# Optimization experiments

Hardware: AMD Instinct MI355X
Metric: run time of the kernel (lower is better)

## Reference

```python
import jax, jax.numpy as jnp
from jax import lax
import numpy as np


def setup_inputs() -> dict:
    key = jax.random.key(0)
    k1, k2 = jax.random.split(key)
    x = jax.random.normal(k1, (128, 256, 3), dtype=jnp.float32)
    y = jax.random.normal(k2, (128, 256, 3), dtype=jnp.float32)
    return {"x": x, "y": y}


def _frechet(x, y):
    B, n, _ = x.shape
    m = y.shape[1]
    INF = jnp.float32(jnp.inf)
    # pairwise squared-distance cost: (B, n, m)
    cost = jnp.sum((x[:, :, None, :] - y[:, None, :, :]) ** 2, axis=-1)

    # DP row 0: dist[0,0]=0, dist[0,j>0]=inf
    row0 = jnp.full((B, m + 1), INF, dtype=cost.dtype).at[:, 0].set(0.0)

    def row_step(prev_row, cost_row):
        # prev_row: (B, m+1) = dist[i-1, :]; cost_row: (B, m)
        up = prev_row[:, 1:]     # dist[i-1, j]   for j=1..m -> (B, m)
        diag = prev_row[:, :-1]  # dist[i-1, j-1] -> (B, m)

        def col_step(left, inp):
            c, u, d = inp  # each (B,)
            min_prev = jnp.minimum(jnp.minimum(u, left), d)
            # torch.where(cost > min_prev, cost, min_prev) == max(cost, min_prev)
            val = jnp.maximum(c, min_prev)
            return val, val

        init_left = jnp.full((B,), INF, dtype=cost.dtype)  # dist[i, 0] = inf
        _, vals = lax.scan(col_step, init_left,
                           (cost_row.T, up.T, diag.T))  # vals: (m, B)
        cur_row = jnp.concatenate(
            [jnp.full((B, 1), INF, dtype=cost.dtype), vals.T], axis=1)
        return cur_row, None

    last_row, _ = lax.scan(row_step, row0, jnp.moveaxis(cost, 1, 0))
    return last_row[:, -1]  # dist[:, n, m] -> (B,)


def reference(x, y):
    return _frechet(x, y)
```

## Files before the change

### kernel.cpp

```cpp
#include <hip/hip_runtime.h>

#define N 256
#define LANES 64
#define NPAIRS 264
#define PPAD   64

typedef float f32x2 __attribute__((ext_vector_type(2)));
typedef float f32x4 __attribute__((ext_vector_type(4)));

__device__ __forceinline__ float dpp_shr1_inf(float v) {
    return __int_as_float(__builtin_amdgcn_update_dpp(
        0x7f800000, __float_as_int(v), 0x138 , 0xf, 0xf, false));
}

__global__ __launch_bounds__(64) void frechet_lin(
    const float* __restrict__ x,
    const float* __restrict__ y,
    float* __restrict__ out)
{
    const int b = blockIdx.x;
    const int t = threadIdx.x;

    const float INF = __builtin_inff();

    __shared__ f32x4 ldsY[2 * NPAIRS];

    {
        const f32x4 pad0 = {0.0f, 0.0f, 0.0f, 0.0f};
        const f32x4 pad1 = {0.0f, 0.0f, INF, INF};
        ldsY[2 * t]     = pad0;
        ldsY[2 * t + 1] = pad1;
        for (int pp = 192 + t; pp < NPAIRS; pp += 64) {
            ldsY[2 * pp]     = pad0;
            ldsY[2 * pp + 1] = pad1;
        }
    }

    #pragma unroll
    for (int k = 0; k < 2; ++k) {
        const int pr = t + 64 * k;
        const int base = (b * N + 2 * pr) * 3;
        const float a0x = y[base + 0], a0y = y[base + 1], a0z = y[base + 2];
        const float a1x = y[base + 3], a1y = y[base + 4], a1z = y[base + 5];
        const float ss0 = a0x*a0x + a0y*a0y + a0z*a0z;
        const float ss1 = a1x*a1x + a1y*a1y + a1z*a1z;
        const int p = pr + PPAD;
        const f32x4 w0 = {a0x, a1x, a0y, a1y};
        const f32x4 w1 = {a0z, a1z, ss0, ss1};
        ldsY[2 * p]     = w0;
        ldsY[2 * p + 1] = w1;
    }

    f32x2 xp0[4], xp1[4], xp2[4], sxp[4];
    #pragma unroll
    for (int r = 0; r < 4; ++r) {
        const float a0 = x[(b * N + 4 * t + r) * 3 + 0];
        const float a1 = x[(b * N + 4 * t + r) * 3 + 1];
        const float a2 = x[(b * N + 4 * t + r) * 3 + 2];
        const float m0 = -2.0f * a0, m1 = -2.0f * a1, m2 = -2.0f * a2;
        const float s  = a0 * a0 + a1 * a1 + a2 * a2;
        xp0[r].x = m0; xp0[r].y = m0;
        xp1[r].x = m1; xp1[r].y = m1;
        xp2[r].x = m2; xp2[r].y = m2;
        sxp[r].x = s;  sxp[r].y = s;
    }
    __syncthreads();

    float lv0 = INF, lv1 = INF, lv2 = INF, lv3 = INF;
    float cb0 = INF, cb1 = INF;
    float diagv = (t == 0) ? 0.0f : INF;

    #define STEP(Q0, Q1)                                                          \
    {                                                                             \
        const float u0 = dpp_shr1_inf(cb0);                                       \
        const float u1 = dpp_shr1_inf(cb1);                                       \
        const f32x2 y0p = (Q0).xy, y1p = (Q0).zw;                                 \
        const f32x2 y2p = (Q1).xy, sab = (Q1).zw;                                 \
        const f32x2 c0p = __builtin_elementwise_fma(xp0[0], y0p,                  \
                          __builtin_elementwise_fma(xp1[0], y1p,                  \
                          __builtin_elementwise_fma(xp2[0], y2p, sxp[0] + sab))); \
        const f32x2 c1p = __builtin_elementwise_fma(xp0[1], y0p,                  \
                          __builtin_elementwise_fma(xp1[1], y1p,                  \
                          __builtin_elementwise_fma(xp2[1], y2p, sxp[1] + sab))); \
        const f32x2 c2p = __builtin_elementwise_fma(xp0[2], y0p,                  \
                          __builtin_elementwise_fma(xp1[2], y1p,                  \
                          __builtin_elementwise_fma(xp2[2], y2p, sxp[2] + sab))); \
        const f32x2 c3p = __builtin_elementwise_fma(xp0[3], y0p,                  \
                          __builtin_elementwise_fma(xp1[3], y1p,                  \
                          __builtin_elementwise_fma(xp2[3], y2p, sxp[3] + sab))); \
        const float v0 = fmaxf(c0p.x, fminf(fminf(u0, lv0), diagv));              \
        const float v1 = fmaxf(c1p.x, fminf(fminf(v0, lv1), lv0));                \
        const float v2 = fmaxf(c2p.x, fminf(fminf(v1, lv2), lv1));                \
        const float v3 = fmaxf(c3p.x, fminf(fminf(v2, lv3), lv2));                \
        const float w0 = fmaxf(c0p.y, fminf(fminf(u1, v0), u0));                  \
        const float w1 = fmaxf(c1p.y, fminf(fminf(w0, v1), v0));                  \
        const float w2 = fmaxf(c2p.y, fminf(fminf(w1, v2), v1));                  \
        const float w3 = fmaxf(c3p.y, fminf(fminf(w2, v3), v2));                  \
        lv0 = w0; lv1 = w1; lv2 = w2; lv3 = w3;                                   \
        cb0 = v3; cb1 = w3;                                                       \
        diagv = u1;                                                               \
    }

    const int q0 = PPAD - t;
    const f32x4* bp = &ldsY[2 * q0];
    f32x4 yA0 = bp[0], yA1 = bp[1];
    f32x4 yB0 = bp[2], yB1 = bp[3];
    f32x4 yC0 = bp[4], yC1 = bp[5];
    bp += 6;

    #pragma unroll 3
    for (int k = 0; k < 63; ++k) {
        STEP(yA0, yA1); yA0 = bp[0]; yA1 = bp[1];
        STEP(yB0, yB1); yB0 = bp[2]; yB1 = bp[3];
        STEP(yC0, yC1); yC0 = bp[4]; yC1 = bp[5];
        bp += 6;
    }
    STEP(yA0, yA1);
    STEP(yB0, yB1);

    #undef STEP

    if (t == LANES - 1)
        out[b] = cb1;
}

extern "C" void kernel_launch(void* const* d_in, const int* in_sizes, int n_in,
                              void* d_out, int out_size, void* d_ws, size_t ws_size,
                              hipStream_t stream) {
    const float* x = (const float*)d_in[0];
    const float* y = (const float*)d_in[1];
    float* out = (float*)d_out;

    const int B = in_sizes[0] / (N * 3);
    frechet_lin<<<B, LANES, 0, stream>>>(x, y, out);
}
```

Measured before the change: 21.38 us.

## Split Frechet DP into forward and reverse wavefronts meeting at anti-diagonal

```diff
diff --git a/kernel.cpp b/kernel.cpp
--- a/kernel.cpp
+++ b/kernel.cpp
@@ -2,8 +2,9 @@
 
 #define N 256
 #define LANES 64
-#define NPAIRS 264
-#define PPAD   64
+#define FRONT 128
+#define NPAIRS 260
+#define NSTEP 128
 
 typedef float f32x2 __attribute__((ext_vector_type(2)));
 typedef float f32x4 __attribute__((ext_vector_type(4)));
@@ -13,50 +14,62 @@
         0x7f800000, __float_as_int(v), 0x138 , 0xf, 0xf, false));
 }
 
-__global__ __launch_bounds__(64) void frechet_lin(
+__global__ __launch_bounds__(128) void frechet_bidir(
     const float* __restrict__ x,
     const float* __restrict__ y,
     float* __restrict__ out)
 {
-    const int b = blockIdx.x;
-    const int t = threadIdx.x;
+    const int b   = blockIdx.x;
+    const int tid = threadIdx.x;
+    const int wid = tid >> 6;
+    const int t   = tid & 63;
 
     const float INF = __builtin_inff();
 
-    __shared__ f32x4 ldsY[2 * NPAIRS];
+    __shared__ f32x4 ldsY[2][2 * NPAIRS];
+    __shared__ float Fd253[256], Fd254[256], Rd254[256], Rd255[256];
+
+    f32x4* reg = ldsY[wid];
 
     {
         const f32x4 pad0 = {0.0f, 0.0f, 0.0f, 0.0f};
         const f32x4 pad1 = {0.0f, 0.0f, INF, INF};
-        ldsY[2 * t]     = pad0;
-        ldsY[2 * t + 1] = pad1;
-        for (int pp = 192 + t; pp < NPAIRS; pp += 64) {
-            ldsY[2 * pp]     = pad0;
-            ldsY[2 * pp + 1] = pad1;
+        reg[2 * t]            = pad0;  reg[2 * t + 1]            = pad1;
+        reg[2 * (t + 64)]     = pad0;  reg[2 * (t + 64) + 1]     = pad1;
+        if (t < 4) {
+            const int pp = FRONT + 128 + t;
+            reg[2 * pp] = pad0;  reg[2 * pp + 1] = pad1;
         }
     }
 
     #pragma unroll
     for (int k = 0; k < 2; ++k) {
         const int pr = t + 64 * k;
-        const int base = (b * N + 2 * pr) * 3;
-        const float a0x = y[base + 0], a0y = y[base + 1], a0z = y[base + 2];
-        const float a1x = y[base + 3], a1y = y[base + 4], a1z = y[base + 5];
+        const int c0 = 2 * pr, c1 = 2 * pr + 1;
+        const int oc0 = wid ? (255 - c0) : c0;
+        const int oc1 = wid ? (255 - c1) : c1;
+        const float a0x = y[(b * N + oc0) * 3 + 0];
+        const float a0y = y[(b * N + oc0) * 3 + 1];
+        const float a0z = y[(b * N + oc0) * 3 + 2];
+        const float a1x = y[(b * N + oc1) * 3 + 0];
+        const float a1y = y[(b * N + oc1) * 3 + 1];
+        const float a1z = y[(b * N + oc1) * 3 + 2];
         const float ss0 = a0x*a0x + a0y*a0y + a0z*a0z;
         const float ss1 = a1x*a1x + a1y*a1y + a1z*a1z;
-        const int p = pr + PPAD;
+        const int p = FRONT + pr;
         const f32x4 w0 = {a0x, a1x, a0y, a1y};
         const f32x4 w1 = {a0z, a1z, ss0, ss1};
-        ldsY[2 * p]     = w0;
-        ldsY[2 * p + 1] = w1;
+        reg[2 * p]     = w0;
+        reg[2 * p + 1] = w1;
     }
 
     f32x2 xp0[4], xp1[4], xp2[4], sxp[4];
     #pragma unroll
     for (int r = 0; r < 4; ++r) {
-        const float a0 = x[(b * N + 4 * t + r) * 3 + 0];
-        const float a1 = x[(b * N + 4 * t + r) * 3 + 1];
-        const float a2 = x[(b * N + 4 * t + r) * 3 + 2];
+        const int orow = wid ? (255 - (4 * t + r)) : (4 * t + r);
+        const float a0 = x[(b * N + orow) * 3 + 0];
+        const float a1 = x[(b * N + orow) * 3 + 1];
+        const float a2 = x[(b * N + orow) * 3 + 2];
         const float m0 = -2.0f * a0, m1 = -2.0f * a1, m2 = -2.0f * a2;
         const float s  = a0 * a0 + a1 * a1 + a2 * a2;
         xp0[r].x = m0; xp0[r].y = m0;
@@ -67,61 +80,97 @@
     __syncthreads();
 
     float lv0 = INF, lv1 = INF, lv2 = INF, lv3 = INF;
-    float cb0 = INF, cb1 = INF;
+    float g0 = INF, g1 = INF;
+    float h0 = INF, h1 = INF;
     float diagv = (t == 0) ? 0.0f : INF;
+    float V0, V1, V2, V3, W0, W1, W2, W3;
 
-    #define STEP(Q0, Q1)                                                          \
-    {                                                                             \
-        const float u0 = dpp_shr1_inf(cb0);                                       \
-        const float u1 = dpp_shr1_inf(cb1);                                       \
-        const f32x2 y0p = (Q0).xy, y1p = (Q0).zw;                                 \
-        const f32x2 y2p = (Q1).xy, sab = (Q1).zw;                                 \
-        const f32x2 c0p = __builtin_elementwise_fma(xp0[0], y0p,                  \
-                          __builtin_elementwise_fma(xp1[0], y1p,                  \
+    #define STEP(Q0v, Q1v, Y0, Y1)                                            \
+    {                                                                         \
+        const float u0 = dpp_shr1_inf(Q0v);                                   \
+        const float u1 = dpp_shr1_inf(Q1v);                                   \
+        const f32x2 y0p = (Y0).xy, y1p = (Y0).zw;                             \
+        const f32x2 y2p = (Y1).xy, sab = (Y1).zw;                             \
+        const f32x2 c0p = __builtin_elementwise_fma(xp0[0], y0p,              \
+                          __builtin_elementwise_fma(xp1[0], y1p,              \
                           __builtin_elementwise_fma(xp2[0], y2p, sxp[0] + sab))); \
-        const f32x2 c1p = __builtin_elementwise_fma(xp0[1], y0p,                  \
-                          __builtin_elementwise_fma(xp1[1], y1p,                  \
+        const f32x2 c1p = __builtin_elementwise_fma(xp0[1], y0p,              \
+                          __builtin_elementwise_fma(xp1[1], y1p,              \
                           __builtin_elementwise_fma(xp2[1], y2p, sxp[1] + sab))); \
-        const f32x2 c2p = __builtin_elementwise_fma(xp0[2], y0p,                  \
-                          __builtin_elementwise_fma(xp1[2], y1p,                  \
+        const f32x2 c2p = __builtin_elementwise_fma(xp0[2], y0p,              \
+                          __builtin_elementwise_fma(xp1[2], y1p,              \
                           __builtin_elementwise_fma(xp2[2], y2p, sxp[2] + sab))); \
-        const f32x2 c3p = __builtin_elementwise_fma(xp0[3], y0p,                  \
-                          __builtin_elementwise_fma(xp1[3], y1p,                  \
+        const f32x2 c3p = __builtin_elementwise_fma(xp0[3], y0p,              \
+                          __builtin_elementwise_fma(xp1[3], y1p,              \
                           __builtin_elementwise_fma(xp2[3], y2p, sxp[3] + sab))); \
-        const float v0 = fmaxf(c0p.x, fminf(fminf(u0, lv0), diagv));              \
-        const float v1 = fmaxf(c1p.x, fminf(fminf(v0, lv1), lv0));                \
-        const float v2 = fmaxf(c2p.x, fminf(fminf(v1, lv2), lv1));                \
-        const float v3 = fmaxf(c3p.x, fminf(fminf(v2, lv3), lv2));                \
-        const float w0 = fmaxf(c0p.y, fminf(fminf(u1, v0), u0));                  \
-        const float w1 = fmaxf(c1p.y, fminf(fminf(w0, v1), v0));                  \
-        const float w2 = fmaxf(c2p.y, fminf(fminf(w1, v2), v1));                  \
-        const float w3 = fmaxf(c3p.y, fminf(fminf(w2, v3), v2));                  \
-        lv0 = w0; lv1 = w1; lv2 = w2; lv3 = w3;                                   \
-        cb0 = v3; cb1 = w3;                                                       \
-        diagv = u1;                                                               \
+        V0 = fmaxf(c0p.x, fminf(fminf(u0, lv0), diagv));                      \
+        V1 = fmaxf(c1p.x, fminf(fminf(V0, lv1), lv0));                        \
+        V2 = fmaxf(c2p.x, fminf(fminf(V1, lv2), lv1));                        \
+        V3 = fmaxf(c3p.x, fminf(fminf(V2, lv3), lv2));                        \
+        W0 = fmaxf(c0p.y, fminf(fminf(u1, V0), u0));                          \
+        W1 = fmaxf(c1p.y, fminf(fminf(W0, V1), V0));                          \
+        W2 = fmaxf(c2p.y, fminf(fminf(W1, V2), V1));                          \
+        W3 = fmaxf(c3p.y, fminf(fminf(W2, V3), V2));                          \
+        lv0 = W0; lv1 = W1; lv2 = W2; lv3 = W3;                               \
+        Q0v = V3; Q1v = W3;                                                   \
+        diagv = u1;                                                           \
     }
 
-    const int q0 = PPAD - t;
-    const f32x4* bp = &ldsY[2 * q0];
+    const int q0 = FRONT - 2 * t;
+    const f32x4* bp = &reg[2 * q0];
     f32x4 yA0 = bp[0], yA1 = bp[1];
     f32x4 yB0 = bp[2], yB1 = bp[3];
     f32x4 yC0 = bp[4], yC1 = bp[5];
     bp += 6;
 
-    #pragma unroll 3
-    for (int k = 0; k < 63; ++k) {
-        STEP(yA0, yA1); yA0 = bp[0]; yA1 = bp[1];
-        STEP(yB0, yB1); yB0 = bp[2]; yB1 = bp[3];
-        STEP(yC0, yC1); yC0 = bp[4]; yC1 = bp[5];
-        bp += 6;
+    #pragma unroll 1
+    for (int k = 0; k < 20; ++k) {
+        STEP(g0, g1, yA0, yA1); yA0 = bp[0];  yA1 = bp[1];
+        STEP(h0, h1, yB0, yB1); yB0 = bp[2];  yB1 = bp[3];
+        STEP(g0, g1, yC0, yC1); yC0 = bp[4];  yC1 = bp[5];
+        STEP(h0, h1, yA0, yA1); yA0 = bp[6];  yA1 = bp[7];
+        STEP(g0, g1, yB0, yB1); yB0 = bp[8];  yB1 = bp[9];
+        STEP(h0, h1, yC0, yC1); yC0 = bp[10]; yC1 = bp[11];
+        bp += 12;
     }
-    STEP(yA0, yA1);
-    STEP(yB0, yB1);
+    STEP(g0, g1, yA0, yA1); yA0 = bp[0]; yA1 = bp[1];
+    STEP(h0, h1, yB0, yB1); yB0 = bp[2]; yB1 = bp[3];
+    STEP(g0, g1, yC0, yC1); yC0 = bp[4]; yC1 = bp[5];
+    STEP(h0, h1, yA0, yA1); yA0 = bp[6]; yA1 = bp[7];
+    STEP(g0, g1, yB0, yB1); yB0 = bp[8]; yB1 = bp[9];
+    STEP(h0, h1, yC0, yC1);
+    if (wid == 0) { Fd253[4*t+2] = W2; Fd253[4*t+3] = V3; Fd254[4*t+3] = W3; }
+    else          { Rd254[4*t+3] = W3; }
+    STEP(g0, g1, yA0, yA1);
+    if (wid == 0) { Fd253[4*t]   = W0; Fd253[4*t+1] = V1;
+                    Fd254[4*t+1] = W1; Fd254[4*t+2] = V2; }
+    else          { Rd255[4*t+2] = W2; Rd255[4*t+3] = V3;
+                    Rd254[4*t+1] = W1; Rd254[4*t+2] = V2; }
+    STEP(h0, h1, yB0, yB1);
+    if (wid == 0) { Fd254[4*t]   = V0; }
+    else          { Rd255[4*t]   = W0; Rd255[4*t+1] = V1; Rd254[4*t] = V0; }
 
     #undef STEP
 
-    if (t == LANES - 1)
-        out[b] = cb1;
+    __syncthreads();
+
+    if (wid == 0) {
+        float m = INF;
+        #pragma unroll
+        for (int k = 0; k < 4; ++k) {
+            const int r  = 4 * t + k;
+            const int i2 = (254 - r) < 0 ? 0 : (254 - r);
+            const float rn = Rd255[i2];
+            const float ta = fmaxf(Fd254[r],
+                                   fminf(fminf(Rd255[255 - r], rn), Rd254[i2]));
+            const float tb = fmaxf(Fd253[r], rn);
+            m = fminf(m, fminf(ta, tb));
+        }
+        #pragma unroll
+        for (int off = 32; off >= 1; off >>= 1)
+            m = fminf(m, __shfl_xor(m, off));
+        if (t == 0) out[b] = m;
+    }
 }
 
 extern "C" void kernel_launch(void* const* d_in, const int* in_sizes, int n_in,
@@ -132,5 +181,5 @@
     float* out = (float*)d_out;
 
     const int B = in_sizes[0] / (N * 3);
-    frechet_lin<<<B, LANES, 0, stream>>>(x, y, out);
+    frechet_bidir<<<B, 128, 0, stream>>>(x, y, out);
 }
```

After: 17.50 us, median of 2. -18.2%, faster.
